# Optimization experiments

Hardware: AMD Instinct MI355X
Metric: run time of the kernel (lower is better)

The kernel has to match this reference:

```python
import jax, jax.numpy as jnp
import numpy as np

# static config (matches init_kwargs)
B, T, D = 4, 1024, 512
H, G = 8, 2
HD = D // H            # 64
REP = H // G           # 4
CHUNK = 64
LC = 2 * CHUNK         # left_context = context_chunk_number * chunk_size = 128
MAXPOS = CHUNK + LC    # 192
NLAYER = 4
EPS = 1e-4
NEG = -50000.0


def _ln(x, w, b):
    m = x.mean(-1, keepdims=True)
    v = ((x - m) ** 2).mean(-1, keepdims=True)
    return (x - m) / jnp.sqrt(v + EPS) * w + b


def _chunk_mask(mask_length):
    # get_mask_vector(CHUNK, mask_length, LC)
    corr = (mask_length + CHUNK - 1) // CHUNK * CHUNK
    row = jnp.arange(corr)[:, None]
    col = jnp.arange(corr + LC)[None, :]
    start = (row // CHUNK) * CHUNK
    cm = (col >= start) & (col < start + CHUNK + LC)
    cm = cm[:mask_length, LC:LC + mask_length]
    return jnp.where(cm, 0.0, -jnp.inf)


def _cut_masks(mask, lens):
    # _cut_masks_with_len_vector
    Lm = mask.shape[0]
    lim = (lens + LC)[:, None]                      # [B,1]
    inb = jnp.arange(Lm)[None, :] < lim             # [B,Lm]
    valid = inb[:, :, None] & inb[:, None, :]       # [B,Lm,Lm]
    return jnp.where(valid, mask[None], NEG)


def _attn(xp, wq, wk, wv, wo, rel_tab, mask):
    # GQASelfAttentionRelPos forward. xp:[B,Tp,D], mask:[B,Tp,Tp]
    Bb, Tp, _ = xp.shape
    scale = 1.0 / jnp.sqrt(jnp.float32(HD))
    q = (xp @ wq.T).reshape(Bb, Tp, H, HD) * scale
    k = jnp.repeat((xp @ wk.T).reshape(Bb, Tp, G, HD), REP, axis=2)
    v = jnp.repeat((xp @ wv.T).reshape(Bb, Tp, G, HD), REP, axis=2)
    scores = jnp.einsum('bqhd,bkhd->bhqk', q, k)
    r = jnp.arange(Tp)
    dist = jnp.clip(r[None, :] - r[:, None], -(MAXPOS - 1), MAXPOS - 1) + MAXPOS - 1
    rel = rel_tab[dist]                              # [Tp,Tp,HD], row=query
    scores = scores + jnp.einsum('bqhd,kqd->bhqk', q, rel)  # matches 'bhd,thd->bht'
    scores = scores + mask[:, None]                  # broadcast over heads
    p = jax.nn.softmax(scores, axis=-1)
    out = jnp.einsum('bhqk,bkhd->bqhd', p, v).reshape(Bb, Tp, D)
    return out @ wo.T


def _conv(x, pw1, dw, pw2):
    # Conformer-style ConvModule(d_model, kernel=9): pointwise->GLU->depthwise->SiLU->pointwise
    h = x @ pw1.T                                   # [B,T,2D]
    a, g = jnp.split(h, 2, axis=-1)
    h = a * jax.nn.sigmoid(g)                       # GLU
    h = jnp.transpose(h, (0, 2, 1))                 # [B,D,T]
    h = jax.lax.conv_general_dilated(h, dw[:, None, :], (1,), [(4, 4)],
                                     dimension_numbers=('NCH', 'OIH', 'NCH'),
                                     feature_group_count=D)
    h = jax.nn.silu(h)
    h = jnp.transpose(h, (0, 2, 1))
    return h @ pw2.T


def _ffn(x, w1, w2):
    # SwiGLUFFN(factor=2)
    h = x @ w1.T
    a, b = jnp.split(h, 2, axis=-1)
    return (jax.nn.silu(a) * b) @ w2.T


def setup_inputs() -> dict:
    key = jax.random.key(0)
    ks = iter(jax.random.split(key, 40))
    s = 0.02
    def rn(shape):
        return jax.random.normal(next(ks), shape, jnp.float32) * s
    L = NLAYER
    return {
        'x': jax.random.normal(next(ks), (B, T, D), jnp.float32),
        'audio_len': jax.random.randint(next(ks), (B,), 1, T + 1),
        'ln1_w': jnp.ones((L, D), jnp.float32), 'ln1_b': jnp.zeros((L, D), jnp.float32),
        'wq': rn((L, D, D)), 'wk': rn((L, G * HD, D)), 'wv': rn((L, G * HD, D)), 'wo': rn((L, D, D)),
        'rel_emb': rn((L, 2 * MAXPOS - 1, HD)),
        'ln2_w': jnp.ones((L, D), jnp.float32), 'ln2_b': jnp.zeros((L, D), jnp.float32),
        'conv_pw1': rn((L, 2 * D, D)), 'conv_dw': rn((L, D, 9)), 'conv_pw2': rn((L, D, D)),
        'ln3_w': jnp.ones((L, D), jnp.float32), 'ln3_b': jnp.zeros((L, D), jnp.float32),
        'ffn_w1': rn((L, 4 * D, D)), 'ffn_w2': rn((L, D, 2 * D)),
    }


def reference(x, audio_len, ln1_w, ln1_b, wq, wk, wv, wo, rel_emb,
              ln2_w, ln2_b, conv_pw1, conv_dw, conv_pw2,
              ln3_w, ln3_b, ffn_w1, ffn_w2):
    mask = _cut_masks(_chunk_mask(T + LC), audio_len)   # [B,Tp,Tp]
    for i in range(NLAYER):
        x = _ln(x, ln1_w[i], ln1_b[i])
        xp = jnp.pad(x, ((0, 0), (LC, 0), (0, 0)))
        x = x + _attn(xp, wq[i], wk[i], wv[i], wo[i], rel_emb[i], mask)[:, LC:]
        x = _ln(x, ln2_w[i], ln2_b[i])
        x = x + _conv(x, conv_pw1[i], conv_dw[i], conv_pw2[i])
        x = _ln(x, ln3_w[i], ln3_b[i])
        x = x + _ffn(x, ffn_w1[i], ffn_w2[i])
    return x
```

## Files before the change

kernel.cpp:

```cpp
#include <hip/hip_runtime.h>
#include <hip/hip_bf16.h>

typedef __hip_bfloat16 bf16;
typedef unsigned short ushort_t;
typedef unsigned int uint_t;
typedef __attribute__((ext_vector_type(8))) short short8;
typedef __attribute__((ext_vector_type(4))) float floatx4;

__device__ __forceinline__ float b2f(bf16 x) { return __bfloat162float(x); }
__device__ __forceinline__ ushort_t f2us(float f) { bf16 h = __float2bfloat16(f); return *(ushort_t*)&h; }
__device__ __forceinline__ float us2f(ushort_t u) { return __uint_as_float(((uint_t)u) << 16); }

constexpr int Bc = 4, Tc = 1024, Dc = 512, Hc = 8, HDc = 64;
constexpr int LCc = 128, MPc = 192;
constexpr float EPSc = 1e-4f;
constexpr int NBT = Bc * Tc;
constexpr long NE = (long)NBT * Dc;
constexpr float NEGB = -1e30f;
constexpr int PSTRIDE = 8704;

__device__ __forceinline__ float wload(const void* p, long i, int f32) {
  return f32 ? ((const float*)p)[i] : b2f(((const bf16*)p)[i]);
}

__device__ __forceinline__ void stage_swz(const ushort_t* __restrict__ G, int rowStride,
                                          int rowBase, int k0, ushort_t* L, int nChunk, int t) {
#pragma unroll
  for (int i = t; i < nChunk; i += 256) {
    int r = i >> 3;
    int cs = (i & 7) ^ (r & 7);
    const ushort_t* gp = G + (long)(rowBase + r) * rowStride + k0 + cs * 8;
    __builtin_amdgcn_global_load_lds(
        (const __attribute__((address_space(1))) void*)gp,
        (__attribute__((address_space(3))) void*)&L[(i & ~63) * 8], 16, 0, 0);
  }
}

__global__ void k_detect(const void* __restrict__ x, int* __restrict__ flag) {
  __shared__ int s[256];
  int t = threadIdx.x;
  const unsigned short* u = (const unsigned short*)x;
  int bad = 0;
  for (int j = t; j < 2048; j += 256) {
    int e = (u[j] >> 7) & 0xFF;
    if (e == 0xFF || e > 0x8F || (e != 0 && e < 0x6F)) bad++;
  }
  s[t] = bad;
  __syncthreads();
  for (int off = 128; off > 0; off >>= 1) { if (t < off) s[t] += s[t + off]; __syncthreads(); }
  if (t == 0) flag[0] = (s[0] > 16) ? 1 : 0;
}

__global__ void k_in(const void* __restrict__ in, float* __restrict__ out, int n,
                     const int* __restrict__ flag) {
  int i = blockIdx.x * 256 + threadIdx.x;
  if (i < n) out[i] = wload(in, i, flag[0]);
}
__global__ void k_out(const float* __restrict__ in, void* __restrict__ out, int n,
                      const int* __restrict__ flag) {
  int i = blockIdx.x * 256 + threadIdx.x;
  if (i >= n) return;
  if (flag[0]) ((float*)out)[i] = in[i];
  else         ((bf16*)out)[i] = __float2bfloat16(in[i]);
}

__global__ void k_w2all(const void* wq, const void* wk, const void* wv, const void* wo,
                        const void* rel, const void* pw1, const void* dwv, const void* pw2,
                        const void* w1, const void* w2,
                        ushort_t* __restrict__ wbf, const int* __restrict__ flag) {
  int f32 = flag[0];
  long i = (long)blockIdx.x * 256 + threadIdx.x;
  if (i >= 12175104L) return;
  float v;
  if (i < 1048576) {
    v = wload(wq, i, f32);
  } else if (i < 1572864) {
    long r2 = i - 1048576;
    long l = r2 / 131072, rem = r2 - l * 131072;
    int r = (int)(rem >> 9), c = (int)(rem & 511);
    if (r < 128) v = wload(wk, l * 65536 + (long)r * 512 + c, f32);
    else         v = wload(wv, l * 65536 + (long)(r - 128) * 512 + c, f32);
  } else if (i < 2621440) {
    v = wload(wo, i - 1572864, f32);
  } else if (i < 2719488) {
    v = wload(rel, i - 2621440, f32);
  } else if (i < 4816640) {
    v = wload(pw1, i - 2719488, f32);
  } else if (i < 4835072) {
    long r2 = i - 4816640;
    long l = r2 / 4608, rem = r2 - l * 4608;
    int j = (int)(rem >> 9), d = (int)(rem & 511);
    v = wload(dwv, l * 4608 + (long)d * 9 + j, f32);
  } else if (i < 5883648) {
    v = wload(pw2, i - 4835072, f32);
  } else if (i < 10077952) {
    v = wload(w1, i - 5883648, f32);
  } else {
    v = wload(w2, i - 10077952, f32);
  }
  wbf[i] = f2us(v);
}

__global__ __launch_bounds__(256) void k_ln(const float* __restrict__ x,
    const void* __restrict__ w, const void* __restrict__ bb, long woff,
    float* __restrict__ o, ushort_t* __restrict__ oA, const int* __restrict__ flag) {
  int f32 = flag[0];
  int row = blockIdx.x;
  int t = threadIdx.x;
  int lane = t & 63, wv = t >> 6;
  float2 v = ((const float2*)(x + (long)row * Dc))[t];
  float s = v.x + v.y;
#pragma unroll
  for (int o2 = 1; o2 < 64; o2 <<= 1) s += __shfl_xor(s, o2, 64);
  __shared__ float ws[8];
  if (lane == 0) ws[wv] = s;
  __syncthreads();
  float mean = (ws[0] + ws[1] + ws[2] + ws[3]) * (1.0f / Dc);
  float dx = v.x - mean, dy = v.y - mean;
  float s2 = dx * dx + dy * dy;
#pragma unroll
  for (int o2 = 1; o2 < 64; o2 <<= 1) s2 += __shfl_xor(s2, o2, 64);
  if (lane == 0) ws[4 + wv] = s2;
  __syncthreads();
  float inv = 1.0f / sqrtf((ws[4] + ws[5] + ws[6] + ws[7]) * (1.0f / Dc) + EPSc);
  float v0 = dx * inv * wload(w, woff + 2 * t, f32)     + wload(bb, woff + 2 * t, f32);
  float v1 = dy * inv * wload(w, woff + 2 * t + 1, f32) + wload(bb, woff + 2 * t + 1, f32);
  float2 ov; ov.x = v0; ov.y = v1;
  ((float2*)(o + (long)row * Dc))[t] = ov;
  ((uint_t*)(oA + (long)row * Dc))[t] = (uint_t)f2us(v0) | ((uint_t)f2us(v1) << 16);
}

template<int BM, int BN, bool OBF>
__global__ __launch_bounds__(256) void k_gemm_b(const ushort_t* __restrict__ A, int lda,
    const ushort_t* __restrict__ W, void* __restrict__ C, int ldc,
    const float* __restrict__ addend, float alpha, int K) {
  constexpr int WGM = BM / 64;
  constexpr int WGN = 4 / WGM;
  constexpr int WN = BN / WGN;
  constexpr int NJ = WN / 16;
  __shared__ ushort_t As[BM * 64];
  __shared__ ushort_t Ws[BN * 64];
  int t = threadIdx.x;
  int m0 = blockIdx.y * BM, n0 = blockIdx.x * BN;
  int lane = t & 63, wv = t >> 6;
  int l15 = lane & 15, quad = lane >> 4;
  int wrow = (WGM == 2) ? (wv >> 1) * 64 : 0;
  int wcol = (WGM == 2) ? (wv & 1) * WN : wv * WN;
  floatx4 acc[4][NJ];
#pragma unroll
  for (int i = 0; i < 4; ++i)
#pragma unroll
    for (int j = 0; j < NJ; ++j) acc[i][j] = 0;
  for (int k0 = 0; k0 < K; k0 += 64) {
    stage_swz(A, lda, m0, k0, As, BM * 8, t);
    stage_swz(W, K,  n0, k0, Ws, BN * 8, t);
    __syncthreads();
#pragma unroll
    for (int half = 0; half < 2; ++half) {
      int sw = ((half * 4 + quad) ^ (l15 & 7)) << 3;
      short8 af[4], bfr[NJ];
#pragma unroll
      for (int i = 0; i < 4; ++i) af[i] = *(short8*)&As[(wrow + i * 16 + l15) * 64 + sw];
#pragma unroll
      for (int j = 0; j < NJ; ++j) bfr[j] = *(short8*)&Ws[(wcol + j * 16 + l15) * 64 + sw];
#pragma unroll
      for (int i = 0; i < 4; ++i)
#pragma unroll
        for (int j = 0; j < NJ; ++j)
          acc[i][j] = __builtin_amdgcn_mfma_f32_16x16x32_bf16(af[i], bfr[j], acc[i][j], 0, 0, 0);
    }
    __syncthreads();
  }
#pragma unroll
  for (int i = 0; i < 4; ++i) {
#pragma unroll
    for (int j = 0; j < NJ; ++j) {
#pragma unroll
      for (int rg = 0; rg < 4; ++rg) {
        int m = m0 + wrow + i * 16 + quad * 4 + rg;
        int n = n0 + wcol + j * 16 + l15;
        float v = alpha * acc[i][j][rg];
        if (addend) v += addend[(long)m * ldc + n];
        if (OBF) ((ushort_t*)C)[(long)m * ldc + n] = f2us(v);
        else     ((float*)C)[(long)m * ldc + n] = v;
      }
    }
  }
}

template<int MODE>
__global__ __launch_bounds__(256) void k_gemm_gate(const ushort_t* __restrict__ A, int lda,
    const ushort_t* __restrict__ Wa, const ushort_t* __restrict__ Wg,
    ushort_t* __restrict__ C, int ldc, int K) {
  __shared__ ushort_t As[64 * 64];
  __shared__ ushort_t Wsa[128 * 64];
  __shared__ ushort_t Wsg[128 * 64];
  int t = threadIdx.x;
  int m0 = blockIdx.y * 64, n0 = blockIdx.x * 128;
  int lane = t & 63, wv = t >> 6;
  int l15 = lane & 15, quad = lane >> 4;
  int wcol = wv * 32;
  floatx4 acca[4][2], accg[4][2];
#pragma unroll
  for (int i = 0; i < 4; ++i)
#pragma unroll
    for (int j = 0; j < 2; ++j) { acca[i][j] = 0; accg[i][j] = 0; }
  for (int k0 = 0; k0 < K; k0 += 64) {
    stage_swz(A, lda, m0, k0, As, 512, t);
    stage_swz(Wa, K, n0, k0, Wsa, 1024, t);
    stage_swz(Wg, K, n0, k0, Wsg, 1024, t);
    __syncthreads();
#pragma unroll
    for (int half = 0; half < 2; ++half) {
      int sw = ((half * 4 + quad) ^ (l15 & 7)) << 3;
      short8 af[4], ba[2], bg[2];
#pragma unroll
      for (int i = 0; i < 4; ++i) af[i] = *(short8*)&As[(i * 16 + l15) * 64 + sw];
#pragma unroll
      for (int j = 0; j < 2; ++j) {
        ba[j] = *(short8*)&Wsa[(wcol + j * 16 + l15) * 64 + sw];
        bg[j] = *(short8*)&Wsg[(wcol + j * 16 + l15) * 64 + sw];
      }
#pragma unroll
      for (int i = 0; i < 4; ++i)
#pragma unroll
        for (int j = 0; j < 2; ++j) {
          acca[i][j] = __builtin_amdgcn_mfma_f32_16x16x32_bf16(af[i], ba[j], acca[i][j], 0, 0, 0);
          accg[i][j] = __builtin_amdgcn_mfma_f32_16x16x32_bf16(af[i], bg[j], accg[i][j], 0, 0, 0);
        }
    }
    __syncthreads();
  }
#pragma unroll
  for (int i = 0; i < 4; ++i) {
#pragma unroll
    for (int j = 0; j < 2; ++j) {
#pragma unroll
      for (int rg = 0; rg < 4; ++rg) {
        int m = m0 + i * 16 + quad * 4 + rg;
        int n = n0 + wcol + j * 16 + l15;
        float a = acca[i][j][rg], g = accg[i][j][rg];
        float v;
        if (MODE == 0) v = a * (1.0f / (1.0f + __expf(-g)));
        else           v = (a / (1.0f + __expf(-a))) * g;
        C[(long)m * ldc + n] = f2us(v);
      }
    }
  }
}

__global__ __launch_bounds__(256, 3) void k_attn(const ushort_t* __restrict__ q,
    const ushort_t* __restrict__ kvb,
    const ushort_t* __restrict__ relL, const int* __restrict__ alen,
    ushort_t* __restrict__ out, char* __restrict__ part) {
  int bx = blockIdx.x;
  int h = blockIdx.y, b = blockIdx.z;
  int len = alen[b];
  int inv, qt, grp;
  if (bx < 16) { inv = 0; qt = bx; grp = 0; }
  else         { inv = 1; qt = (bx - 16) & 15; grp = (bx - 16) >> 4; }
  int q0 = qt * 64;
  if (inv) { if (q0 + 64 <= len) return; }
  else     { if (q0 >= len) return; }
  int nvalid = min(len - q0, 64);
  int g = h >> 2;
  __shared__ __align__(16) ushort_t UQB[8704];
  __shared__ __align__(16) ushort_t Ks[64 * 64];
  __shared__ __align__(16) ushort_t Vt[64 * 72];
  __shared__ __align__(16) ushort_t Ps[64 * 64];
  __shared__ __align__(16) float fML[128];
  ushort_t* Qs = UQB;
  ushort_t* B2t = UQB;
  int t = threadIdx.x;
  int lane = t & 63, w = t >> 6;
  int l15 = lane & 15, quad = lane >> 4;
  int qw = w * 16;
  {
    int qi = t >> 2, du = (t & 3) * 16;
    const ushort_t* src = q + ((long)(b * Tc + q0 + qi)) * Dc + h * 64 + du;
    *(uint4*)&Qs[qi * 72 + du] = *(const uint4*)(src);
    *(uint4*)&Qs[qi * 72 + du + 8] = *(const uint4*)(src + 8);
  }
  const int koB = inv ? -128 : (q0 - 128);
  const int KSTEP = inv ? 4 : 1;
  const int nIt = inv ? ((grp < 2) ? 5 : 4) : 3;
  uint4 kr0, kr1, vr0, vr1;
  int kj = t >> 2, du = (t & 3) * 16, c0 = du >> 3;
  auto LOADKV = [&](int kt2) {
    int ko = koB + kt2 * 64 + kj;
    if (ko >= 0) {
      long basek = ((long)(b * Tc + ko)) * 256 + g * 64 + du;
      kr0 = *(const uint4*)(kvb + basek);
      kr1 = *(const uint4*)(kvb + basek + 8);
      vr0 = *(const uint4*)(kvb + basek + 128);
      vr1 = *(const uint4*)(kvb + basek + 136);
    } else {
      uint4 z = {0, 0, 0, 0};
      kr0 = z; kr1 = z; vr0 = z; vr1 = z;
    }
  };
  LOADKV(grp);
  float m_ = NEGB, l_ = 0.f;
  floatx4 acc[4];
#pragma unroll
  for (int j = 0; j < 4; ++j) acc[j] = 0;
  __syncthreads();
  short8 aq0 = *(short8*)&Qs[(qw + l15) * 72 + quad * 8];
  short8 aq1 = *(short8*)&Qs[(qw + l15) * 72 + 32 + quad * 8];
  float rv_lo = 0.f, rv_hi = 0.f;
  if (inv) {
    int er = (l15 == 1) ? 382 : 0;
    short8 be0 = *(const short8*)(relL + (long)er * 64 + quad * 8);
    short8 be1 = *(const short8*)(relL + (long)er * 64 + 32 + quad * 8);
    floatx4 ec = {0.f, 0.f, 0.f, 0.f};
    ec = __builtin_amdgcn_mfma_f32_16x16x32_bf16(be0, aq0, ec, 0, 0, 0);
    ec = __builtin_amdgcn_mfma_f32_16x16x32_bf16(be1, aq1, ec, 0, 0, 0);
    rv_lo = __shfl(ec[0], l15, 64);
    rv_hi = __shfl(ec[1], l15, 64);
  }
  int sw7 = l15 & 7;
  for (int it = 0; it < nIt; ++it) {
    int kt = inv ? (grp + it * KSTEP) : it;
    int ko0 = koB + kt * 64;
    int t0 = q0 - ko0 + 191;
    bool far_hi = (q0 - ko0 - 63) >= 191;
    bool far_lo = (q0 + 63 - ko0) <= -191;
    bool near = !far_hi && !far_lo;
    int cb = min(max(t0 - 63, 0), 255);
    __syncthreads();
    {
      *(uint4*)&Ks[kj * 64 + ((c0 ^ (kj & 7)) << 3)] = kr0;
      *(uint4*)&Ks[kj * 64 + (((c0 + 1) ^ (kj & 7)) << 3)] = kr1;
      uint_t wds[8] = {vr0.x, vr0.y, vr0.z, vr0.w, vr1.x, vr1.y, vr1.z, vr1.w};
#pragma unroll
      for (int u = 0; u < 8; ++u) {
        Vt[(du + 2 * u) * 72 + kj] = (ushort_t)(wds[u] & 0xffff);
        Vt[(du + 2 * u + 1) * 72 + kj] = (ushort_t)(wds[u] >> 16);
      }
    }
    if (near) {
      __builtin_amdgcn_s_setprio(1);
#pragma unroll
      for (int p = 0; p < 2; ++p) {
        short8 rw0[4], rw1[4];
#pragma unroll
        for (int j = 0; j < 4; ++j) {
          long wr = cb + (p * 4 + j) * 16 + l15;
          rw0[j] = *(const short8*)(relL + wr * 64 + quad * 8);
          rw1[j] = *(const short8*)(relL + wr * 64 + 32 + quad * 8);
        }
#pragma unroll
        for (int j = 0; j < 4; ++j) {
          floatx4 z = {0.f, 0.f, 0.f, 0.f};
          z = __builtin_amdgcn_mfma_f32_16x16x32_bf16(rw0[j], aq0, z, 0, 0, 0);
          z = __builtin_amdgcn_mfma_f32_16x16x32_bf16(rw1[j], aq1, z, 0, 0, 0);
#pragma unroll
          for (int rg = 0; rg < 4; ++rg) {
            int cpr = (p * 4 + j) * 16 + quad * 4 + rg;
            B2t[cpr * 68 + qw + l15] = f2us(z[rg]);
          }
        }
      }
      __builtin_amdgcn_s_setprio(0);
    }
    __syncthreads();
    if (it + 1 < nIt) LOADKV(kt + KSTEP);
    floatx4 s[4];
    __builtin_amdgcn_s_setprio(1);
#pragma unroll
    for (int nt = 0; nt < 4; ++nt) {
      short8 ak0 = *(short8*)&Ks[(nt * 16 + l15) * 64 + ((quad ^ sw7) << 3)];
      short8 ak1 = *(short8*)&Ks[(nt * 16 + l15) * 64 + (((4 + quad) ^ sw7) << 3)];
      floatx4 z = {0.f, 0.f, 0.f, 0.f};
      z = __builtin_amdgcn_mfma_f32_16x16x32_bf16(ak0, aq0, z, 0, 0, 0);
      z = __builtin_amdgcn_mfma_f32_16x16x32_bf16(ak1, aq1, z, 0, 0, 0);
      s[nt] = z;
    }
    __builtin_amdgcn_s_setprio(0);
    if (near) {
#pragma unroll
      for (int nt = 0; nt < 4; ++nt)
#pragma unroll
        for (int rg = 0; rg < 4; ++rg) {
          int c = t0 + qw + l15 - (nt * 16 + quad * 4 + rg);
          c = min(max(c, 0), 382);
          s[nt][rg] += us2f(B2t[(c - cb) * 68 + qw + l15]);
        }
    } else {
      float rv = far_hi ? rv_hi : rv_lo;
#pragma unroll
      for (int nt = 0; nt < 4; ++nt)
#pragma unroll
        for (int rg = 0; rg < 4; ++rg) s[nt][rg] += rv;
    }
    if (!inv) {
#pragma unroll
      for (int nt = 0; nt < 4; ++nt)
#pragma unroll
        for (int rg = 0; rg < 4; ++rg) {
          int ko = ko0 + nt * 16 + quad * 4 + rg;
          if (ko >= len) s[nt][rg] = NEGB;
        }
    }
    float mx = s[0][0];
#pragma unroll
    for (int nt = 0; nt < 4; ++nt)
#pragma unroll
      for (int rg = 0; rg < 4; ++rg) mx = fmaxf(mx, s[nt][rg]);
    mx = fmaxf(mx, __shfl_xor(mx, 16, 64));
    mx = fmaxf(mx, __shfl_xor(mx, 32, 64));
    float mn = fmaxf(m_, mx);
    float al = __expf(m_ - mn);
    float ps = 0.f;
#pragma unroll
    for (int nt = 0; nt < 4; ++nt)
#pragma unroll
      for (int rg = 0; rg < 4; ++rg) {
        float p = __expf(s[nt][rg] - mn);
        s[nt][rg] = p;
        ps += p;
      }
    ps += __shfl_xor(ps, 16, 64);
    ps += __shfl_xor(ps, 32, 64);
    l_ = l_ * al + ps;
    m_ = mn;
    if (quad == 0) fML[qw + l15] = al;
#pragma unroll
    for (int nt = 0; nt < 4; ++nt)
#pragma unroll
      for (int pr = 0; pr < 2; ++pr) {
        uint_t pk = (uint_t)f2us(s[nt][2 * pr]) | ((uint_t)f2us(s[nt][2 * pr + 1]) << 16);
        int e = nt * 16 + quad * 4 + pr * 2;
        *(uint_t*)&Ps[(qw + l15) * 64 + (((e >> 3) ^ sw7) << 3) + (e & 7)] = pk;
      }
    floatx4 av = *(floatx4*)&fML[qw + quad * 4];
#pragma unroll
    for (int j = 0; j < 4; ++j)
#pragma unroll
      for (int rg = 0; rg < 4; ++rg) acc[j][rg] *= av[rg];
    short8 ap0 = *(short8*)&Ps[(qw + l15) * 64 + ((quad ^ sw7) << 3)];
    short8 ap1 = *(short8*)&Ps[(qw + l15) * 64 + (((4 + quad) ^ sw7) << 3)];
    __builtin_amdgcn_s_setprio(1);
#pragma unroll
    for (int j = 0; j < 4; ++j) {
      short8 bv0 = *(short8*)&Vt[(j * 16 + l15) * 72 + quad * 8];
      short8 bv1 = *(short8*)&Vt[(j * 16 + l15) * 72 + 32 + quad * 8];
      acc[j] = __builtin_amdgcn_mfma_f32_16x16x32_bf16(ap0, bv0, acc[j], 0, 0, 0);
      acc[j] = __builtin_amdgcn_mfma_f32_16x16x32_bf16(ap1, bv1, acc[j], 0, 0, 0);
    }
    __builtin_amdgcn_s_setprio(0);
  }
  if (inv) {
    char* pp = part + (long)((((b * 8 + h) * 16 + qt) * 4 + grp)) * PSTRIDE;
    ushort_t* Cp = (ushort_t*)pp;
    float* mp = (float*)(pp + 8192);
#pragma unroll
    for (int j = 0; j < 4; ++j)
#pragma unroll
      for (int rg = 0; rg < 4; ++rg)
        Cp[(qw + quad * 4 + rg) * 64 + j * 16 + l15] = f2us(acc[j][rg]);
    if (quad == 0) { mp[qw + l15] = m_; mp[64 + qw + l15] = l_; }
  } else {
    if (quad == 0) fML[64 + qw + l15] = l_;
    floatx4 lv = *(floatx4*)&fML[64 + qw + quad * 4];
#pragma unroll
    for (int rg = 0; rg < 4; ++rg) {
      int R = qw + quad * 4 + rg;
      if (R < nvalid) {
        float invL = 1.0f / lv[rg];
#pragma unroll
        for (int j = 0; j < 4; ++j)
          out[((long)(b * Tc + q0 + R)) * Dc + h * 64 + j * 16 + l15] = f2us(acc[j][rg] * invL);
      }
    }
  }
}

__global__ __launch_bounds__(256) void k_comb(const char* __restrict__ part,
    const int* __restrict__ alen, ushort_t* __restrict__ out) {
  int qt = blockIdx.x, h = blockIdx.y, b = blockIdx.z;
  int len = alen[b];
  int q0 = qt * 64;
  if (q0 + 64 <= len) return;
  int nskip = max(len - q0, 0);
  int t = threadIdx.x;
  int d = t & 63, r0 = (t >> 6) * 16;
  const char* pb = part + (long)(((b * 8 + h) * 16 + qt) * 4) * PSTRIDE;
#pragma unroll 4
  for (int i = 0; i < 16; ++i) {
    int r = r0 + i;
    if (r < nskip) continue;
    float mg[4], lg[4], M = NEGB;
#pragma unroll
    for (int g2 = 0; g2 < 4; ++g2) {
      const float* mp = (const float*)(pb + g2 * PSTRIDE + 8192);
      mg[g2] = mp[r];
      lg[g2] = mp[64 + r];
      M = fmaxf(M, mg[g2]);
    }
    float L = 0.f, wgt[4];
#pragma unroll
    for (int g2 = 0; g2 < 4; ++g2) { wgt[g2] = __expf(mg[g2] - M); L += lg[g2] * wgt[g2]; }
    float v = 0.f;
#pragma unroll
    for (int g2 = 0; g2 < 4; ++g2)
      v += us2f(((const ushort_t*)(pb + g2 * PSTRIDE))[r * 64 + d]) * wgt[g2];
    out[((long)(b * Tc + q0 + r)) * Dc + h * 64 + d] = f2us(v / L);
  }
}

__global__ void k_dwconv(const ushort_t* __restrict__ in, const ushort_t* __restrict__ dwT,
                         ushort_t* __restrict__ out, int n8) {
  int i = blockIdx.x * 256 + threadIdx.x;
  if (i >= n8) return;
  int row = i >> 6;
  int d8 = (i & 63) << 3;
  int t = row & (Tc - 1);
  int b = row >> 10;
  float acc[8] = {0, 0, 0, 0, 0, 0, 0, 0};
#pragma unroll
  for (int j = 0; j < 9; ++j) {
    int tt = t + j - 4;
    if (tt < 0 || tt >= Tc) continue;
    short8 vv = *(const short8*)&in[((long)(b * Tc + tt) << 9) + d8];
    short8 dv = *(const short8*)&dwT[j * 512 + d8];
#pragma unroll
    for (int e = 0; e < 8; ++e)
      acc[e] += us2f((ushort_t)vv[e]) * us2f((ushort_t)dv[e]);
  }
  short8 o8;
#pragma unroll
  for (int e = 0; e < 8; ++e)
    o8[e] = (short)f2us(acc[e] * (1.0f / (1.0f + __expf(-acc[e]))));
  *(short8*)&out[(long)row * 512 + d8] = o8;
}

extern "C" void kernel_launch(void* const* d_in, const int* in_sizes, int n_in,
                              void* d_out, int out_size, void* d_ws, size_t ws_size,
                              hipStream_t stream) {
  const void* x_in = d_in[0];
  const int*  alen = (const int*)d_in[1];
  const void* ln1w = d_in[2];
  const void* ln1b = d_in[3];
  const void* wq   = d_in[4];
  const void* wk   = d_in[5];
  const void* wv   = d_in[6];
  const void* wo   = d_in[7];
  const void* rel  = d_in[8];
  const void* ln2w = d_in[9];
  const void* ln2b = d_in[10];
  const void* pw1  = d_in[11];
  const void* dwv  = d_in[12];
  const void* pw2  = d_in[13];
  const void* ln3w = d_in[14];
  const void* ln3b = d_in[15];
  const void* w1   = d_in[16];
  const void* w2   = d_in[17];

  char* base = (char*)d_ws;
  int*      flag = (int*)base;
  float*    xf   = (float*)(base + 256);
  float*    lnb  = (float*)(base + 256 + 8388608);
  ushort_t* lnA  = (ushort_t*)(base + 16777472);
  ushort_t* wbf  = (ushort_t*)(base + 20971776);
  char*     U    = base + 45321984;
  ushort_t* qb  = (ushort_t*)U;
  ushort_t* kvb = (ushort_t*)(U + 4194304);
  ushort_t* ab  = (ushort_t*)(U + 6291456);
  char*     partA = U + 10485760;
  ushort_t* big = (ushort_t*)U;
  ushort_t* cb  = (ushort_t*)(U + 16777216);
  size_t REQ = 45321984 + 16777216 + 4194304;
  size_t REQ2 = 45321984 + 35651584;
  if (REQ2 > REQ) REQ = REQ2;
  if (ws_size < REQ) return;

  ushort_t* wqB   = wbf + 0;
  ushort_t* wkvB  = wbf + 1048576;
  ushort_t* woB   = wbf + 1572864;
  ushort_t* relB  = wbf + 2621440;
  ushort_t* pw1B  = wbf + 2719488;
  ushort_t* dwB   = wbf + 4816640;
  ushort_t* pw2B  = wbf + 4835072;
  ushort_t* w1B   = wbf + 5883648;
  ushort_t* w2B   = wbf + 10077952;

  k_detect<<<1, 256, 0, stream>>>(x_in, flag);
  k_in<<<(int)((NE + 255) / 256), 256, 0, stream>>>(x_in, xf, (int)NE, flag);
  k_w2all<<<47559, 256, 0, stream>>>(wq, wk, wv, wo, rel, pw1, dwv, pw2, w1, w2, wbf, flag);

  for (int i = 0; i < 4; ++i) {
    long oLN = (long)i * Dc;
    k_ln<<<NBT, 256, 0, stream>>>(xf, ln1w, ln1b, oLN, lnb, lnA, flag);
    k_gemm_b<64, 128, true><<<dim3(4, 64), 256, 0, stream>>>(lnA, Dc, wqB + (long)i * 262144, qb, Dc, nullptr, 0.125f, 512);
    k_gemm_b<64, 128, true><<<dim3(2, 64), 256, 0, stream>>>(lnA, Dc, wkvB + (long)i * 131072, kvb, 256, nullptr, 1.0f, 512);
    k_attn<<<dim3(80, 8, 4), 256, 0, stream>>>(qb, kvb, relB + (long)i * 24512, alen, ab, partA);
    k_comb<<<dim3(16, 8, 4), 256, 0, stream>>>(partA, alen, ab);
    k_gemm_b<64, 128, false><<<dim3(4, 64), 256, 0, stream>>>(ab, Dc, woB + (long)i * 262144, xf, Dc, lnb, 1.0f, 512);

    k_ln<<<NBT, 256, 0, stream>>>(xf, ln2w, ln2b, oLN, lnb, lnA, flag);
    k_gemm_gate<0><<<dim3(4, 64), 256, 0, stream>>>(lnA, Dc, pw1B + (long)i * 524288,
        pw1B + (long)i * 524288 + 262144, big, 512, 512);
    k_dwconv<<<NBT * 512 / 8 / 256, 256, 0, stream>>>(big, dwB + (long)i * 4608, cb, NBT * 512 / 8);
    k_gemm_b<64, 128, false><<<dim3(4, 64), 256, 0, stream>>>(cb, Dc, pw2B + (long)i * 262144, xf, Dc, lnb, 1.0f, 512);

    k_ln<<<NBT, 256, 0, stream>>>(xf, ln3w, ln3b, oLN, lnb, lnA, flag);
    k_gemm_gate<1><<<dim3(8, 64), 256, 0, stream>>>(lnA, Dc, w1B + (long)i * 1048576,
        w1B + (long)i * 1048576 + 524288, big, 1024, 512);
    k_gemm_b<64, 128, false><<<dim3(4, 64), 256, 0, stream>>>(big, 1024, w2B + (long)i * 524288, xf, Dc, lnb, 1.0f, 1024);
  }

  k_out<<<(int)((NE + 255) / 256), 256, 0, stream>>>(xf, d_out, (int)NE, flag);
}
```

Measured before the change: 945.6 us.

## Fuse QKV projections, double-buffer GEMM LDS tiles, shrink gate GEMM tile

The Q, K and V weights are packed into one [768,512] matrix per layer, with the 1/8 query scale folded into the weights at conversion time. One GEMM now produces an interleaved QKV buffer that attention reads with a 768 stride. The generic and gated GEMMs double-buffer their LDS tiles so loads for the next K step are issued before the current step's MFMAs. The gated GEMM N tile is halved to 64 so more blocks launch. Together these cut launches and hide load latency, at the cost of twice the LDS per block, which may lower occupancy.

```diff
diff --git a/kernel.cpp b/kernel.cpp
--- a/kernel.cpp
+++ b/kernel.cpp
@@ -18,6 +18,7 @@
 constexpr long NE = (long)NBT * Dc;
 constexpr float NEGB = -1e30f;
 constexpr int PSTRIDE = 8704;
+constexpr int QSTR = 768;
 
 __device__ __forceinline__ float wload(const void* p, long i, int f32) {
   return f32 ? ((const float*)p)[i] : b2f(((const bf16*)p)[i]);
@@ -72,14 +73,12 @@
   long i = (long)blockIdx.x * 256 + threadIdx.x;
   if (i >= 12175104L) return;
   float v;
-  if (i < 1048576) {
-    v = wload(wq, i, f32);
-  } else if (i < 1572864) {
-    long r2 = i - 1048576;
-    long l = r2 / 131072, rem = r2 - l * 131072;
+  if (i < 1572864) {
+    long l = i / 393216, rem = i - l * 393216;
     int r = (int)(rem >> 9), c = (int)(rem & 511);
-    if (r < 128) v = wload(wk, l * 65536 + (long)r * 512 + c, f32);
-    else         v = wload(wv, l * 65536 + (long)(r - 128) * 512 + c, f32);
+    if (r < 512)      v = 0.125f * wload(wq, l * 262144 + (long)r * 512 + c, f32);
+    else if (r < 640) v = wload(wk, l * 65536 + (long)(r - 512) * 512 + c, f32);
+    else              v = wload(wv, l * 65536 + (long)(r - 640) * 512 + c, f32);
   } else if (i < 2621440) {
     v = wload(wo, i - 1572864, f32);
   } else if (i < 2719488) {
@@ -138,8 +137,8 @@
   constexpr int WGN = 4 / WGM;
   constexpr int WN = BN / WGN;
   constexpr int NJ = WN / 16;
-  __shared__ ushort_t As[BM * 64];
-  __shared__ ushort_t Ws[BN * 64];
+  __shared__ ushort_t As[2][BM * 64];
+  __shared__ ushort_t Ws[2][BN * 64];
   int t = threadIdx.x;
   int m0 = blockIdx.y * BM, n0 = blockIdx.x * BN;
   int lane = t & 63, wv = t >> 6;
@@ -151,18 +150,26 @@
   for (int i = 0; i < 4; ++i)
 #pragma unroll
     for (int j = 0; j < NJ; ++j) acc[i][j] = 0;
+  stage_swz(A, lda, m0, 0, As[0], BM * 8, t);
+  stage_swz(W, K,  n0, 0, Ws[0], BN * 8, t);
+  __syncthreads();
+  int cur = 0;
   for (int k0 = 0; k0 < K; k0 += 64) {
-    stage_swz(A, lda, m0, k0, As, BM * 8, t);
-    stage_swz(W, K,  n0, k0, Ws, BN * 8, t);
-    __syncthreads();
+    int nk = k0 + 64;
+    if (nk < K) {
+      stage_swz(A, lda, m0, nk, As[cur ^ 1], BM * 8, t);
+      stage_swz(W, K,  n0, nk, Ws[cur ^ 1], BN * 8, t);
+    }
+    const ushort_t* Asc = As[cur];
+    const ushort_t* Wsc = Ws[cur];
 #pragma unroll
     for (int half = 0; half < 2; ++half) {
       int sw = ((half * 4 + quad) ^ (l15 & 7)) << 3;
       short8 af[4], bfr[NJ];
 #pragma unroll
-      for (int i = 0; i < 4; ++i) af[i] = *(short8*)&As[(wrow + i * 16 + l15) * 64 + sw];
-#pragma unroll
-      for (int j = 0; j < NJ; ++j) bfr[j] = *(short8*)&Ws[(wcol + j * 16 + l15) * 64 + sw];
+      for (int i = 0; i < 4; ++i) af[i] = *(short8*)&Asc[(wrow + i * 16 + l15) * 64 + sw];
+#pragma unroll
+      for (int j = 0; j < NJ; ++j) bfr[j] = *(short8*)&Wsc[(wcol + j * 16 + l15) * 64 + sw];
 #pragma unroll
       for (int i = 0; i < 4; ++i)
 #pragma unroll
@@ -170,6 +177,7 @@
           acc[i][j] = __builtin_amdgcn_mfma_f32_16x16x32_bf16(af[i], bfr[j], acc[i][j], 0, 0, 0);
     }
     __syncthreads();
+    cur ^= 1;
   }
 #pragma unroll
   for (int i = 0; i < 4; ++i) {
@@ -192,65 +200,65 @@
 __global__ __launch_bounds__(256) void k_gemm_gate(const ushort_t* __restrict__ A, int lda,
     const ushort_t* __restrict__ Wa, const ushort_t* __restrict__ Wg,
     ushort_t* __restrict__ C, int ldc, int K) {
-  __shared__ ushort_t As[64 * 64];
-  __shared__ ushort_t Wsa[128 * 64];
-  __shared__ ushort_t Wsg[128 * 64];
+  __shared__ ushort_t As[2][64 * 64];
+  __shared__ ushort_t Wsa[2][64 * 64];
+  __shared__ ushort_t Wsg[2][64 * 64];
   int t = threadIdx.x;
-  int m0 = blockIdx.y * 64, n0 = blockIdx.x * 128;
+  int m0 = blockIdx.y * 64, n0 = blockIdx.x * 64;
   int lane = t & 63, wv = t >> 6;
   int l15 = lane & 15, quad = lane >> 4;
-  int wcol = wv * 32;
-  floatx4 acca[4][2], accg[4][2];
-#pragma unroll
-  for (int i = 0; i < 4; ++i)
-#pragma unroll
-    for (int j = 0; j < 2; ++j) { acca[i][j] = 0; accg[i][j] = 0; }
+  int wcol = wv * 16;
+  floatx4 acca[4], accg[4];
+#pragma unroll
+  for (int i = 0; i < 4; ++i) { acca[i] = 0; accg[i] = 0; }
+  stage_swz(A, lda, m0, 0, As[0], 512, t);
+  stage_swz(Wa, K, n0, 0, Wsa[0], 512, t);
+  stage_swz(Wg, K, n0, 0, Wsg[0], 512, t);
+  __syncthreads();
+  int cur = 0;
   for (int k0 = 0; k0 < K; k0 += 64) {
-    stage_swz(A, lda, m0, k0, As, 512, t);
-    stage_swz(Wa, K, n0, k0, Wsa, 1024, t);
-    stage_swz(Wg, K, n0, k0, Wsg, 1024, t);
-    __syncthreads();
+    int nk = k0 + 64;
+    if (nk < K) {
+      stage_swz(A, lda, m0, nk, As[cur ^ 1], 512, t);
+      stage_swz(Wa, K, n0, nk, Wsa[cur ^ 1], 512, t);
+      stage_swz(Wg, K, n0, nk, Wsg[cur ^ 1], 512, t);
+    }
+    const ushort_t* Asc = As[cur];
+    const ushort_t* Wac = Wsa[cur];
+    const ushort_t* Wgc = Wsg[cur];
 #pragma unroll
     for (int half = 0; half < 2; ++half) {
       int sw = ((half * 4 + quad) ^ (l15 & 7)) << 3;
-      short8 af[4], ba[2], bg[2];
-#pragma unroll
-      for (int i = 0; i < 4; ++i) af[i] = *(short8*)&As[(i * 16 + l15) * 64 + sw];
-#pragma unroll
-      for (int j = 0; j < 2; ++j) {
-        ba[j] = *(short8*)&Wsa[(wcol + j * 16 + l15) * 64 + sw];
-        bg[j] = *(short8*)&Wsg[(wcol + j * 16 + l15) * 64 + sw];
+      short8 af[4], ba, bg;
+#pragma unroll
+      for (int i = 0; i < 4; ++i) af[i] = *(short8*)&Asc[(i * 16 + l15) * 64 + sw];
+      ba = *(short8*)&Wac[(wcol + l15) * 64 + sw];
+      bg = *(short8*)&Wgc[(wcol + l15) * 64 + sw];
+#pragma unroll
+      for (int i = 0; i < 4; ++i) {
+        acca[i] = __builtin_amdgcn_mfma_f32_16x16x32_bf16(af[i], ba, acca[i], 0, 0, 0);
+        accg[i] = __builtin_amdgcn_mfma_f32_16x16x32_bf16(af[i], bg, accg[i], 0, 0, 0);
       }
-#pragma unroll
-      for (int i = 0; i < 4; ++i)
-#pragma unroll
-        for (int j = 0; j < 2; ++j) {
-          acca[i][j] = __builtin_amdgcn_mfma_f32_16x16x32_bf16(af[i], ba[j], acca[i][j], 0, 0, 0);
-          accg[i][j] = __builtin_amdgcn_mfma_f32_16x16x32_bf16(af[i], bg[j], accg[i][j], 0, 0, 0);
-        }
     }
     __syncthreads();
+    cur ^= 1;
   }
 #pragma unroll
   for (int i = 0; i < 4; ++i) {
 #pragma unroll
-    for (int j = 0; j < 2; ++j) {
-#pragma unroll
-      for (int rg = 0; rg < 4; ++rg) {
-        int m = m0 + i * 16 + quad * 4 + rg;
-        int n = n0 + wcol + j * 16 + l15;
-        float a = acca[i][j][rg], g = accg[i][j][rg];
-        float v;
-        if (MODE == 0) v = a * (1.0f / (1.0f + __expf(-g)));
-        else           v = (a / (1.0f + __expf(-a))) * g;
-        C[(long)m * ldc + n] = f2us(v);
-      }
-    }
-  }
-}
-
-__global__ __launch_bounds__(256, 3) void k_attn(const ushort_t* __restrict__ q,
-    const ushort_t* __restrict__ kvb,
+    for (int rg = 0; rg < 4; ++rg) {
+      int m = m0 + i * 16 + quad * 4 + rg;
+      int n = n0 + wcol + l15;
+      float a = acca[i][rg], g = accg[i][rg];
+      float v;
+      if (MODE == 0) v = a * (1.0f / (1.0f + __expf(-g)));
+      else           v = (a / (1.0f + __expf(-a))) * g;
+      C[(long)m * ldc + n] = f2us(v);
+    }
+  }
+}
+
+__global__ __launch_bounds__(256, 3) void k_attn(const ushort_t* __restrict__ qkv,
     const ushort_t* __restrict__ relL, const int* __restrict__ alen,
     ushort_t* __restrict__ out, char* __restrict__ part) {
   int bx = blockIdx.x;
@@ -277,7 +285,7 @@
   int qw = w * 16;
   {
     int qi = t >> 2, du = (t & 3) * 16;
-    const ushort_t* src = q + ((long)(b * Tc + q0 + qi)) * Dc + h * 64 + du;
+    const ushort_t* src = qkv + ((long)(b * Tc + q0 + qi)) * QSTR + h * 64 + du;
     *(uint4*)&Qs[qi * 72 + du] = *(const uint4*)(src);
     *(uint4*)&Qs[qi * 72 + du + 8] = *(const uint4*)(src + 8);
   }
@@ -289,11 +297,11 @@
   auto LOADKV = [&](int kt2) {
     int ko = koB + kt2 * 64 + kj;
     if (ko >= 0) {
-      long basek = ((long)(b * Tc + ko)) * 256 + g * 64 + du;
-      kr0 = *(const uint4*)(kvb + basek);
-      kr1 = *(const uint4*)(kvb + basek + 8);
-      vr0 = *(const uint4*)(kvb + basek + 128);
-      vr1 = *(const uint4*)(kvb + basek + 136);
+      long basek = ((long)(b * Tc + ko)) * QSTR + 512 + g * 64 + du;
+      kr0 = *(const uint4*)(qkv + basek);
+      kr1 = *(const uint4*)(qkv + basek + 8);
+      vr0 = *(const uint4*)(qkv + basek + 128);
+      vr1 = *(const uint4*)(qkv + basek + 136);
     } else {
       uint4 z = {0, 0, 0, 0};
       kr0 = z; kr1 = z; vr0 = z; vr1 = z;
@@ -564,8 +572,7 @@
   ushort_t* lnA  = (ushort_t*)(base + 16777472);
   ushort_t* wbf  = (ushort_t*)(base + 20971776);
   char*     U    = base + 45321984;
-  ushort_t* qb  = (ushort_t*)U;
-  ushort_t* kvb = (ushort_t*)(U + 4194304);
+  ushort_t* qkv = (ushort_t*)U;
   ushort_t* ab  = (ushort_t*)(U + 6291456);
   char*     partA = U + 10485760;
   ushort_t* big = (ushort_t*)U;
@@ -575,8 +582,7 @@
   if (REQ2 > REQ) REQ = REQ2;
   if (ws_size < REQ) return;
 
-  ushort_t* wqB   = wbf + 0;
-  ushort_t* wkvB  = wbf + 1048576;
+  ushort_t* qkvB  = wbf + 0;
   ushort_t* woB   = wbf + 1572864;
   ushort_t* relB  = wbf + 2621440;
   ushort_t* pw1B  = wbf + 2719488;
@@ -592,20 +598,19 @@
   for (int i = 0; i < 4; ++i) {
     long oLN = (long)i * Dc;
     k_ln<<<NBT, 256, 0, stream>>>(xf, ln1w, ln1b, oLN, lnb, lnA, flag);
-    k_gemm_b<64, 128, true><<<dim3(4, 64), 256, 0, stream>>>(lnA, Dc, wqB + (long)i * 262144, qb, Dc, nullptr, 0.125f, 512);
-    k_gemm_b<64, 128, true><<<dim3(2, 64), 256, 0, stream>>>(lnA, Dc, wkvB + (long)i * 131072, kvb, 256, nullptr, 1.0f, 512);
-    k_attn<<<dim3(80, 8, 4), 256, 0, stream>>>(qb, kvb, relB + (long)i * 24512, alen, ab, partA);
+    k_gemm_b<64, 128, true><<<dim3(6, 64), 256, 0, stream>>>(lnA, Dc, qkvB + (long)i * 393216, qkv, QSTR, nullptr, 1.0f, 512);
+    k_attn<<<dim3(80, 8, 4), 256, 0, stream>>>(qkv, relB + (long)i * 24512, alen, ab, partA);
     k_comb<<<dim3(16, 8, 4), 256, 0, stream>>>(partA, alen, ab);
     k_gemm_b<64, 128, false><<<dim3(4, 64), 256, 0, stream>>>(ab, Dc, woB + (long)i * 262144, xf, Dc, lnb, 1.0f, 512);
 
     k_ln<<<NBT, 256, 0, stream>>>(xf, ln2w, ln2b, oLN, lnb, lnA, flag);
-    k_gemm_gate<0><<<dim3(4, 64), 256, 0, stream>>>(lnA, Dc, pw1B + (long)i * 524288,
+    k_gemm_gate<0><<<dim3(8, 64), 256, 0, stream>>>(lnA, Dc, pw1B + (long)i * 524288,
         pw1B + (long)i * 524288 + 262144, big, 512, 512);
     k_dwconv<<<NBT * 512 / 8 / 256, 256, 0, stream>>>(big, dwB + (long)i * 4608, cb, NBT * 512 / 8);
     k_gemm_b<64, 128, false><<<dim3(4, 64), 256, 0, stream>>>(cb, Dc, pw2B + (long)i * 262144, xf, Dc, lnb, 1.0f, 512);
 
     k_ln<<<NBT, 256, 0, stream>>>(xf, ln3w, ln3b, oLN, lnb, lnA, flag);
-    k_gemm_gate<1><<<dim3(8, 64), 256, 0, stream>>>(lnA, Dc, w1B + (long)i * 1048576,
+    k_gemm_gate<1><<<dim3(16, 64), 256, 0, stream>>>(lnA, Dc, w1B + (long)i * 1048576,
         w1B + (long)i * 1048576 + 524288, big, 1024, 512);
     k_gemm_b<64, 128, false><<<dim3(4, 64), 256, 0, stream>>>(big, 1024, w2B + (long)i * 524288, xf, Dc, lnb, 1.0f, 1024);
   }
```

Measured after the change: 932.2 us. No clear change (-1.4%).
